# Performance work log

Hardware: AMD Instinct MI355X
Metric: run time of the kernel (lower is better)

Reference implementation:

```python
import jax, jax.numpy as jnp
import numpy as np

B, T, F, H = 1024, 256, 23, 100  # batch, timesteps, lab features, LSTM hidden
S_IN, S_OUT = 6, 20              # fc_state: Linear(6, 20)
FC_IN, N_CLS = 120, 2            # fc: Linear(120, 2)


def setup_inputs() -> dict:
    key = jax.random.key(0)
    ks = jax.random.split(key, 10)
    sc = 0.1  # weight init scale
    return {
        "x_lab": jax.random.normal(ks[0], (B, T, F), jnp.float32),
        "t_lab": jax.random.uniform(ks[1], (1, B, T), jnp.float32, minval=0.0, maxval=10.0),
        "x_state": jax.random.normal(ks[2], (B, S_IN), jnp.float32),
        # time-aware LSTM (LSTM2) params
        "W_x": jax.random.normal(ks[3], (F, 4 * H), jnp.float32) * sc,
        "W_h": jax.random.normal(ks[4], (H, 4 * H), jnp.float32) * sc,
        "b_lstm": jnp.zeros((4 * H,), jnp.float32),
        "W_d": jax.random.normal(ks[5], (H, H), jnp.float32) * sc,   # cell-decomposition weight
        "b_d": jnp.zeros((H,), jnp.float32),
        # fc_state: Linear(6, 20)
        "W_state": jax.random.normal(ks[6], (S_IN, S_OUT), jnp.float32) * sc,
        "b_state": jnp.zeros((S_OUT,), jnp.float32),
        # fc: Linear(120, 2)
        "W_fc": jax.random.normal(ks[7], (FC_IN, N_CLS), jnp.float32) * sc,
        "b_fc": jnp.zeros((N_CLS,), jnp.float32),
    }


def reference(x_lab, t_lab, x_state, W_x, W_h, b_lstm, W_d, b_d,
              W_state, b_state, W_fc, b_fc):
    # Time-aware LSTM (T-LSTM style): decompose prev cell into short-term
    # memory, decay it by g(dt) = 1 / log(e + dt), then standard LSTM gates.
    dt = jnp.transpose(t_lab[0])            # [T, B] elapsed-time deltas
    xs = jnp.transpose(x_lab, (1, 0, 2))    # [T, B, F]
    # Precompute input projections for all steps (one big GEMM).
    x_proj = jnp.einsum('tbf,fg->tbg', xs, W_x) + b_lstm  # [T, B, 4H]

    def step(carry, inp):
        h, c = carry                          # [B, H] each
        xp, d = inp                           # [B, 4H], [B]
        c_short = jnp.tanh(c @ W_d + b_d)     # short-term memory
        decay = (1.0 / jnp.log(jnp.e + d))[:, None]
        c_adj = c - c_short + c_short * decay # long-term + decayed short-term
        gates = xp + h @ W_h                  # [B, 4H]
        i, f, g, o = jnp.split(gates, 4, axis=1)
        i = jax.nn.sigmoid(i)
        f = jax.nn.sigmoid(f)
        o = jax.nn.sigmoid(o)
        g = jnp.tanh(g)
        c_new = f * c_adj + i * g
        h_new = o * jnp.tanh(c_new)
        return (h_new, c_new), None

    b = x_lab.shape[0]
    init = (jnp.zeros((b, H), x_lab.dtype), jnp.zeros((b, H), x_lab.dtype))
    (h_final, _), _ = jax.lax.scan(step, init, (x_proj, dt))

    e_state = x_state @ W_state + b_state          # [B, 20]
    y = jnp.concatenate([h_final, e_state], axis=1) @ W_fc + b_fc  # [B, 2]
    return jax.nn.softmax(y, axis=1)
```

## Files before the change

### kernel.cpp

```cpp
#include <hip/hip_runtime.h>

#define TT   256
#define FF   23
#define HH   100
#define NTHR 448
#define NWG  256

typedef unsigned int  u32;
typedef unsigned short u16;
typedef __attribute__((ext_vector_type(8))) short short8;
typedef __attribute__((ext_vector_type(4))) float f32x4;

__device__ __forceinline__ u16 f2bf(float f){
  u32 u = __float_as_uint(f);
  u += 0x7fffu + ((u >> 16) & 1u);
  return (u16)(u >> 16);
}
__device__ __forceinline__ float fsig(float x){
  return __builtin_amdgcn_rcpf(1.0f + __expf(-x));
}
__device__ __forceinline__ float ftanh(float x){
  return 1.0f - 2.0f * __builtin_amdgcn_rcpf(__expf(2.0f * x) + 1.0f);
}


__global__ __launch_bounds__(NTHR, 2) void tlstm9(
    const float* __restrict__ x_lab,  const float* __restrict__ t_lab,
    const float* __restrict__ x_state,const float* __restrict__ W_x,
    const float* __restrict__ W_h,    const float* __restrict__ b_lstm,
    const float* __restrict__ W_d,    const float* __restrict__ b_d,
    const float* __restrict__ W_state,const float* __restrict__ b_state,
    const float* __restrict__ W_fc,   const float* __restrict__ b_fc,
    float* __restrict__ out)
{
  __shared__ __align__(16) u16  sX[TT][128];
  __shared__ __align__(16) u16  sHC[2][2][384];
  __shared__ __align__(16) float sDec[TT][4];
  __shared__ __align__(16) float sHF[4][128];

  const int tid  = threadIdx.x;
  const int lane = tid & 63;
  const int w    = tid >> 6;
  const int nl   = lane & 15;
  const int q4   = lane >> 4;
  const int b0   = blockIdx.x * 4;
  const int j    = w * 16 + nl;
  const bool jr  = (j < HH);

  for (int i = tid; i < 2*2*384/2; i += NTHR) ((u32*)sHC)[i] = 0u;

  for (int e = tid; e < TT*128; e += NTHR) {
    int t = e >> 7, inner = e & 127, r = inner >> 5, k = inner & 31;
    float v = 0.f;
    if (k < FF)       v = x_lab[((b0 + r)*TT + t)*FF + k];
    else if (k == 31) v = 1.0f;
    sX[t][inner] = f2bf(v);
  }
  for (int e = tid; e < TT*4; e += NTHR) {
    int t = e >> 2, r = e & 3;
    sDec[t][r] = 1.0f / logf(2.718281828459045f + t_lab[(b0 + r)*TT + t]);
  }

  short8 wh[4][3], wd[3], wdx, wx[4];
#pragma unroll
  for (int g = 0; g < 4; ++g)
#pragma unroll
    for (int kf = 0; kf < 3; ++kf) {
      short8 v;
#pragma unroll
      for (int i = 0; i < 8; ++i) {
        int k = kf*32 + q4*8 + i;
        v[i] = (short)(jr ? f2bf(W_h[k*400 + g*HH + j]) : 0);
      }
      wh[g][kf] = v;
    }
#pragma unroll
  for (int kf = 0; kf < 3; ++kf) {
    short8 v;
#pragma unroll
    for (int i = 0; i < 8; ++i) {
      int k = kf*32 + q4*8 + i;
      v[i] = (short)(jr ? f2bf(W_d[k*HH + j]) : 0);
    }
    wd[kf] = v;
  }
  {
    short8 v;
#pragma unroll
    for (int i = 0; i < 8; ++i) {
      int k = q4*8 + i;
      float x = 0.f;
      if (jr) {
        if (k >= 27 && k < 31) x = W_d[(96 + (k-27))*HH + j];
        else if (k == 31)      x = b_d[j];
      }
      v[i] = (short)f2bf(x);
    }
    wdx = v;
  }
#pragma unroll
  for (int g = 0; g < 4; ++g) {
    short8 v;
#pragma unroll
    for (int i = 0; i < 8; ++i) {
      int k = q4*8 + i;
      float x = 0.f;
      if (jr) {
        if (k < FF)                 x = W_x[k*400 + g*HH + j];
        else if (k >= 23 && k < 27) x = W_h[(96 + (k-23))*400 + g*HH + j];
        else if (k == 31)           x = b_lstm[g*HH + j];
      }
      v[i] = (short)f2bf(x);
    }
    wx[g] = v;
  }

  __syncthreads();

  const bool rdr   = ((nl & 3) == 0);
  const int  rbase = (nl >> 2)*32 + q4*8;
  const int  widx  = (j >> 5)*128 + q4*32 + (j & 31);
  const bool wbuf  = (w < 6);
  const bool wfold = (w == 6) && (nl < 4);

  float cm = 0.f, hl = 0.f;
  const f32x4 zv = {0.f, 0.f, 0.f, 0.f};

#define MFMA16(a,b,c) __builtin_amdgcn_mfma_f32_16x16x32_bf16(a, b, c, 0, 0, 0)

#define STEP_BODY(T, PC, PN)                                                  \
  {                                                                           \
    const u16* hb = sHC[PC][0];                                               \
    const u16* cb = sHC[PC][1];                                               \
    u16* hn = sHC[PN][0];                                                     \
    u16* cn = sHC[PN][1];                                                     \
    short8 xa={},ha0={},ha1={},ha2={},ca0={},ca1={},ca2={};                   \
    if (rdr) {                                                                \
      ca0 = *(const short8*)(cb +       rbase);                               \
      ca1 = *(const short8*)(cb + 128 + rbase);                               \
      ca2 = *(const short8*)(cb + 256 + rbase);                               \
      xa  = *(const short8*)(sX[T] + rbase);                                  \
      ha0 = *(const short8*)(hb +       rbase);                               \
      ha1 = *(const short8*)(hb + 128 + rbase);                               \
      ha2 = *(const short8*)(hb + 256 + rbase);                               \
    }                                                                         \
    float dec = sDec[T][q4];                                                  \
                      \
    f32x4 d0 = MFMA16(ca0, wd[0], zv), d1 = MFMA16(ca1, wd[1], zv);           \
    d0 = MFMA16(ca2, wd[2], d0);       d1 = MFMA16(xa, wdx, d1);              \
    f32x4 p0[4], p1[4];                                                       \
    _Pragma("unroll")                                                         \
    for (int g = 0; g < 4; ++g) {                                             \
      p0[g] = MFMA16(xa,  wx[g],    zv);                                      \
      p1[g] = MFMA16(ha0, wh[g][0], zv);                                      \
      p0[g] = MFMA16(ha1, wh[g][1], p0[g]);                                   \
      p1[g] = MFMA16(ha2, wh[g][2], p1[g]);                                   \
    }                                                                         \
    float cs   = ftanh(d0[0] + d1[0]);                                        \
    float cadj = cm - cs + cs*dec;                                            \
    float ig = fsig (p0[0][0] + p1[0][0]);                                    \
    float fg = fsig (p0[1][0] + p1[1][0]);                                    \
    float gg = ftanh(p0[2][0] + p1[2][0]);                                    \
    float og = fsig (p0[3][0] + p1[3][0]);                                    \
    float cnv = fg*cadj + ig*gg;  cm = cnv;                                   \
    float hv  = og*ftanh(cnv);    hl = hv;                                    \
    u32 pk;                                                                   \
    asm("v_cvt_pk_bf16_f32 %0, %1, %2" : "=v"(pk) : "v"(hv), "v"(cnv));       \
    if (wbuf) {                                                               \
      hn[widx] = (u16)pk;                                                     \
      cn[widx] = (u16)(pk >> 16);                                             \
    } else if (wfold && (T) + 1 < TT) {                                       \
      sX[(T)+1][q4*32 + 23 + nl] = (u16)pk;                                   \
      sX[(T)+1][q4*32 + 27 + nl] = (u16)(pk >> 16);                           \
    }                                                                         \
    __syncthreads();                                                          \
  }

  for (int t = 0; t < TT; t += 2) {
    STEP_BODY(t,     0, 1)
    STEP_BODY(t + 1, 1, 0)
  }
#undef STEP_BODY
#undef MFMA16

  if (jr) sHF[q4][j] = hl;
  __syncthreads();

  if (tid < 4) {
    const int bg = b0 + tid;
    float y0 = b_fc[0], y1 = b_fc[1];
    for (int k = 0; k < HH; ++k) {
      float hv = sHF[tid][k];
      y0 += hv * W_fc[2*k];
      y1 += hv * W_fc[2*k + 1];
    }
#pragma unroll
    for (int k = 0; k < 20; ++k) {
      float a = b_state[k];
#pragma unroll
      for (int s = 0; s < 6; ++s) a += x_state[bg*6 + s] * W_state[s*20 + k];
      y0 += a * W_fc[2*(HH + k)];
      y1 += a * W_fc[2*(HH + k) + 1];
    }
    float m = fmaxf(y0, y1);
    float e0 = __expf(y0 - m), e1 = __expf(y1 - m);
    float inv = 1.0f / (e0 + e1);
    out[bg*2 + 0] = e0 * inv;
    out[bg*2 + 1] = e1 * inv;
  }
}

extern "C" void kernel_launch(void* const* d_in, const int* in_sizes, int n_in,
                              void* d_out, int out_size, void* d_ws, size_t ws_size,
                              hipStream_t stream) {
  const float* x_lab   = (const float*)d_in[0];
  const float* t_lab   = (const float*)d_in[1];
  const float* x_state = (const float*)d_in[2];
  const float* W_x     = (const float*)d_in[3];
  const float* W_h     = (const float*)d_in[4];
  const float* b_lstm  = (const float*)d_in[5];
  const float* W_d     = (const float*)d_in[6];
  const float* b_d     = (const float*)d_in[7];
  const float* W_state = (const float*)d_in[8];
  const float* b_state = (const float*)d_in[9];
  const float* W_fc    = (const float*)d_in[10];
  const float* b_fc    = (const float*)d_in[11];
  float* outp = (float*)d_out;

  hipLaunchKernelGGL(tlstm9, dim3(NWG), dim3(NTHR), 0, stream,
                     x_lab, t_lab, x_state, W_x, W_h, b_lstm, W_d, b_d,
                     W_state, b_state, W_fc, b_fc, outp);
}
```

Measured before the change: 209.7 us.

## Split K dimension of recurrent MFMAs across two wave groups per step

Doubles the workgroup to 14 waves. Each hidden-column tile's K reduction is split between two waves: group A does x, c0, c1 and h0, while group B does h1, h2 and c2 and writes its partial sums to a new shared buffer. After an extra barrier, group A adds the partials and runs the gate math. The decay is folded to (decay-1) so c_adj becomes a single FMA. This halves the per-wave MFMA chain on the serial critical path, at the cost of a second barrier and a shared-memory round trip each step, and occupancy falls to one workgroup per CU.

```diff
diff --git a/kernel.cpp b/kernel.cpp
--- a/kernel.cpp
+++ b/kernel.cpp
@@ -3,7 +3,7 @@
 #define TT   256
 #define FF   23
 #define HH   100
-#define NTHR 448
+#define NTHR 896
 #define NWG  256
 
 typedef unsigned int  u32;
@@ -24,7 +24,7 @@
 }
 
 
-__global__ __launch_bounds__(NTHR, 2) void tlstm9(
+__global__ __launch_bounds__(NTHR) void tlstm11(
     const float* __restrict__ x_lab,  const float* __restrict__ t_lab,
     const float* __restrict__ x_state,const float* __restrict__ W_x,
     const float* __restrict__ W_h,    const float* __restrict__ b_lstm,
@@ -35,16 +35,19 @@
 {
   __shared__ __align__(16) u16  sX[TT][128];
   __shared__ __align__(16) u16  sHC[2][2][384];
+  __shared__ __align__(16) float sPart[5 * 448];
   __shared__ __align__(16) float sDec[TT][4];
   __shared__ __align__(16) float sHF[4][128];
 
   const int tid  = threadIdx.x;
   const int lane = tid & 63;
   const int w    = tid >> 6;
+  const bool isA = (w < 7);
+  const int wp   = isA ? w : (w - 7);
   const int nl   = lane & 15;
   const int q4   = lane >> 4;
   const int b0   = blockIdx.x * 4;
-  const int j    = w * 16 + nl;
+  const int j    = wp * 16 + nl;
   const bool jr  = (j < HH);
 
   for (int i = tid; i < 2*2*384/2; i += NTHR) ((u32*)sHC)[i] = 0u;
@@ -58,73 +61,85 @@
   }
   for (int e = tid; e < TT*4; e += NTHR) {
     int t = e >> 2, r = e & 3;
-    sDec[t][r] = 1.0f / logf(2.718281828459045f + t_lab[(b0 + r)*TT + t]);
-  }
-
-  short8 wh[4][3], wd[3], wdx, wx[4];
-#pragma unroll
-  for (int g = 0; g < 4; ++g)
-#pragma unroll
-    for (int kf = 0; kf < 3; ++kf) {
-      short8 v;
-#pragma unroll
-      for (int i = 0; i < 8; ++i) {
-        int k = kf*32 + q4*8 + i;
-        v[i] = (short)(jr ? f2bf(W_h[k*400 + g*HH + j]) : 0);
-      }
-      wh[g][kf] = v;
+    sDec[t][r] = 1.0f / logf(2.718281828459045f + t_lab[(b0 + r)*TT + t]) - 1.0f;
+  }
+
+  short8 wt[11];
+#pragma unroll
+  for (int i = 0; i < 11; ++i) wt[i] = short8{0,0,0,0,0,0,0,0};
+  if (jr) {
+    if (isA) {
+#pragma unroll
+      for (int g = 0; g < 4; ++g) {
+        short8 v;
+#pragma unroll
+        for (int i = 0; i < 8; ++i) {
+          int k = q4*8 + i;
+          float x = 0.f;
+          if (k < FF)                 x = W_x[k*400 + g*HH + j];
+          else if (k >= 23 && k < 27) x = W_h[(96 + (k-23))*400 + g*HH + j];
+          else if (k == 31)           x = b_lstm[g*HH + j];
+          v[i] = (short)f2bf(x);
+        }
+        wt[g] = v;
+      }
+      {
+        short8 v;
+#pragma unroll
+        for (int i = 0; i < 8; ++i) {
+          int k = q4*8 + i;
+          float x = 0.f;
+          if (k >= 27 && k < 31) x = W_d[(96 + (k-27))*HH + j];
+          else if (k == 31)      x = b_d[j];
+          v[i] = (short)f2bf(x);
+        }
+        wt[4] = v;
+      }
+#pragma unroll
+      for (int kf = 0; kf < 2; ++kf) {
+        short8 v;
+#pragma unroll
+        for (int i = 0; i < 8; ++i) v[i] = (short)f2bf(W_d[(kf*32 + q4*8 + i)*HH + j]);
+        wt[5 + kf] = v;
+      }
+#pragma unroll
+      for (int g = 0; g < 4; ++g) {
+        short8 v;
+#pragma unroll
+        for (int i = 0; i < 8; ++i) v[i] = (short)f2bf(W_h[(q4*8 + i)*400 + g*HH + j]);
+        wt[7 + g] = v;
+      }
+    } else {
+#pragma unroll
+      for (int g = 0; g < 4; ++g) {
+        short8 v, u;
+#pragma unroll
+        for (int i = 0; i < 8; ++i) {
+          v[i] = (short)f2bf(W_h[(32 + q4*8 + i)*400 + g*HH + j]);
+          u[i] = (short)f2bf(W_h[(64 + q4*8 + i)*400 + g*HH + j]);
+        }
+        wt[g] = v; wt[7 + g] = u;
+      }
+      {
+        short8 v;
+#pragma unroll
+        for (int i = 0; i < 8; ++i) v[i] = (short)f2bf(W_d[(64 + q4*8 + i)*HH + j]);
+        wt[5] = v;
+      }
     }
-#pragma unroll
-  for (int kf = 0; kf < 3; ++kf) {
-    short8 v;
-#pragma unroll
-    for (int i = 0; i < 8; ++i) {
-      int k = kf*32 + q4*8 + i;
-      v[i] = (short)(jr ? f2bf(W_d[k*HH + j]) : 0);
-    }
-    wd[kf] = v;
-  }
-  {
-    short8 v;
-#pragma unroll
-    for (int i = 0; i < 8; ++i) {
-      int k = q4*8 + i;
-      float x = 0.f;
-      if (jr) {
-        if (k >= 27 && k < 31) x = W_d[(96 + (k-27))*HH + j];
-        else if (k == 31)      x = b_d[j];
-      }
-      v[i] = (short)f2bf(x);
-    }
-    wdx = v;
-  }
-#pragma unroll
-  for (int g = 0; g < 4; ++g) {
-    short8 v;
-#pragma unroll
-    for (int i = 0; i < 8; ++i) {
-      int k = q4*8 + i;
-      float x = 0.f;
-      if (jr) {
-        if (k < FF)                 x = W_x[k*400 + g*HH + j];
-        else if (k >= 23 && k < 27) x = W_h[(96 + (k-23))*400 + g*HH + j];
-        else if (k == 31)           x = b_lstm[g*HH + j];
-      }
-      v[i] = (short)f2bf(x);
-    }
-    wx[g] = v;
   }
 
   __syncthreads();
 
-  const bool rdr   = ((nl & 3) == 0);
   const int  rbase = (nl >> 2)*32 + q4*8;
   const int  widx  = (j >> 5)*128 + q4*32 + (j & 31);
-  const bool wbuf  = (w < 6);
-  const bool wfold = (w == 6) && (nl < 4);
+  const int  pidx  = q4*112 + j;
+  const bool wbuf  = (wp < 6);
+  const bool wfold = (wp == 6) && (nl < 4);
 
   float cm = 0.f, hl = 0.f;
   const f32x4 zv = {0.f, 0.f, 0.f, 0.f};
+  float* sP = sPart;
 
 #define MFMA16(a,b,c) __builtin_amdgcn_mfma_f32_16x16x32_bf16(a, b, c, 0, 0, 0)
 
@@ -134,46 +149,65 @@
     const u16* cb = sHC[PC][1];                                               \
     u16* hn = sHC[PN][0];                                                     \
     u16* cn = sHC[PN][1];                                                     \
-    short8 xa={},ha0={},ha1={},ha2={},ca0={},ca1={},ca2={};                   \
-    if (rdr) {                                                                \
-      ca0 = *(const short8*)(cb +       rbase);                               \
-      ca1 = *(const short8*)(cb + 128 + rbase);                               \
-      ca2 = *(const short8*)(cb + 256 + rbase);                               \
-      xa  = *(const short8*)(sX[T] + rbase);                                  \
-      ha0 = *(const short8*)(hb +       rbase);                               \
-      ha1 = *(const short8*)(hb + 128 + rbase);                               \
-      ha2 = *(const short8*)(hb + 256 + rbase);                               \
+    f32x4 acP0, acP1, acP2, acP3, acD0, acD1;                                 \
+    if (isA) {                                                                \
+      short8 f0 = *(const short8*)(sX[T] + rbase);         \
+      short8 f1 = *(const short8*)(cb +       rbase);      \
+      short8 f2 = *(const short8*)(cb + 128 + rbase);      \
+      short8 f3 = *(const short8*)(hb +       rbase);      \
+      acD0 = MFMA16(f0, wt[4], zv);                                           \
+      acP0 = MFMA16(f0, wt[0], zv);                                           \
+      acP1 = MFMA16(f0, wt[1], zv);                                           \
+      acP2 = MFMA16(f0, wt[2], zv);                                           \
+      acP3 = MFMA16(f0, wt[3], zv);                                           \
+      acD0 = MFMA16(f1, wt[5], acD0);                                         \
+      acD1 = MFMA16(f2, wt[6], zv);                                           \
+      acP0 = MFMA16(f3, wt[7],  acP0);                                        \
+      acP1 = MFMA16(f3, wt[8],  acP1);                                        \
+      acP2 = MFMA16(f3, wt[9],  acP2);                                        \
+      acP3 = MFMA16(f3, wt[10], acP3);                                        \
+    } else {                                                                  \
+      short8 f1 = *(const short8*)(hb + 128 + rbase);      \
+      short8 f2 = *(const short8*)(hb + 256 + rbase);      \
+      short8 f3 = *(const short8*)(cb + 256 + rbase);      \
+      acP0 = MFMA16(f1, wt[0], zv);                                           \
+      acP1 = MFMA16(f1, wt[1], zv);                                           \
+      acP2 = MFMA16(f1, wt[2], zv);                                           \
+      acP3 = MFMA16(f1, wt[3], zv);                                           \
+      acD0 = MFMA16(f3, wt[5], zv);                                           \
+      acP0 = MFMA16(f2, wt[7],  acP0);                                        \
+      acP1 = MFMA16(f2, wt[8],  acP1);                                        \
+      acP2 = MFMA16(f2, wt[9],  acP2);                                        \
+      acP3 = MFMA16(f2, wt[10], acP3);                                        \
+      sP[pidx         ] = acP0[0];                                            \
+      sP[pidx +  448  ] = acP1[0];                                            \
+      sP[pidx +  896  ] = acP2[0];                                            \
+      sP[pidx + 1344  ] = acP3[0];                                            \
+      sP[pidx + 1792  ] = acD0[0];                                            \
     }                                                                         \
-    float dec = sDec[T][q4];                                                  \
-                      \
-    f32x4 d0 = MFMA16(ca0, wd[0], zv), d1 = MFMA16(ca1, wd[1], zv);           \
-    d0 = MFMA16(ca2, wd[2], d0);       d1 = MFMA16(xa, wdx, d1);              \
-    f32x4 p0[4], p1[4];                                                       \
-    _Pragma("unroll")                                                         \
-    for (int g = 0; g < 4; ++g) {                                             \
-      p0[g] = MFMA16(xa,  wx[g],    zv);                                      \
-      p1[g] = MFMA16(ha0, wh[g][0], zv);                                      \
-      p0[g] = MFMA16(ha1, wh[g][1], p0[g]);                                   \
-      p1[g] = MFMA16(ha2, wh[g][2], p1[g]);                                   \
+    __syncthreads();                \
+    if (isA) {                                                                \
+      float decm1 = sDec[T][q4];                                              \
+      float ds = acD0[0] + acD1[0] + sP[pidx + 1792];                         \
+      float cs   = ftanh(ds);                                                 \
+      float cadj = __builtin_fmaf(cs, decm1, cm);                             \
+      float ig = fsig (acP0[0] + sP[pidx        ]);                           \
+      float fg = fsig (acP1[0] + sP[pidx +  448 ]);                           \
+      float gg = ftanh(acP2[0] + sP[pidx +  896 ]);                           \
+      float og = fsig (acP3[0] + sP[pidx + 1344 ]);                           \
+      float cnv = fg*cadj + ig*gg;  cm = cnv;                                 \
+      float hv  = og*ftanh(cnv);    hl = hv;                                  \
+      u32 pk;                                                                 \
+      asm("v_cvt_pk_bf16_f32 %0, %1, %2" : "=v"(pk) : "v"(hv), "v"(cnv));     \
+      if (wbuf) {                                                             \
+        hn[widx] = (u16)pk;                                                   \
+        cn[widx] = (u16)(pk >> 16);                                           \
+      } else if (wfold && (T) + 1 < TT) {                                     \
+        sX[(T)+1][q4*32 + 23 + nl] = (u16)pk;                                 \
+        sX[(T)+1][q4*32 + 27 + nl] = (u16)(pk >> 16);                         \
+      }                                                                       \
     }                                                                         \
-    float cs   = ftanh(d0[0] + d1[0]);                                        \
-    float cadj = cm - cs + cs*dec;                                            \
-    float ig = fsig (p0[0][0] + p1[0][0]);                                    \
-    float fg = fsig (p0[1][0] + p1[1][0]);                                    \
-    float gg = ftanh(p0[2][0] + p1[2][0]);                                    \
-    float og = fsig (p0[3][0] + p1[3][0]);                                    \
-    float cnv = fg*cadj + ig*gg;  cm = cnv;                                   \
-    float hv  = og*ftanh(cnv);    hl = hv;                                    \
-    u32 pk;                                                                   \
-    asm("v_cvt_pk_bf16_f32 %0, %1, %2" : "=v"(pk) : "v"(hv), "v"(cnv));       \
-    if (wbuf) {                                                               \
-      hn[widx] = (u16)pk;                                                     \
-      cn[widx] = (u16)(pk >> 16);                                             \
-    } else if (wfold && (T) + 1 < TT) {                                       \
-      sX[(T)+1][q4*32 + 23 + nl] = (u16)pk;                                   \
-      sX[(T)+1][q4*32 + 27 + nl] = (u16)(pk >> 16);                           \
-    }                                                                         \
-    __syncthreads();                                                          \
+    __syncthreads();                                   \
   }
 
   for (int t = 0; t < TT; t += 2) {
@@ -183,7 +217,7 @@
 #undef STEP_BODY
 #undef MFMA16
 
-  if (jr) sHF[q4][j] = hl;
+  if (isA && jr) sHF[q4][j] = hl;
   __syncthreads();
 
   if (tid < 4) {
@@ -227,7 +261,7 @@
   const float* b_fc    = (const float*)d_in[11];
   float* outp = (float*)d_out;
 
-  hipLaunchKernelGGL(tlstm9, dim3(NWG), dim3(NTHR), 0, stream,
+  hipLaunchKernelGGL(tlstm11, dim3(NWG), dim3(NTHR), 0, stream,
                      x_lab, t_lab, x_state, W_x, W_h, b_lstm, W_d, b_d,
                      W_state, b_state, W_fc, b_fc, outp);
 }
```

Result: faster. 195.4 us (-6.8%).
